# Kernel optimization log

Hardware: AMD Instinct MI355X
Metric: run time of the kernel (lower is better)

Reference implementation:

```python
import jax, jax.numpy as jnp
import numpy as np

B, C, NS, NT = 8, 256, 16384, 2048
KQ = 64            # self-attention key/query dim
D = 64             # cond_conv_feat_dim
W0, W1, W2 = D * D, D * D, D * 1   # dynamic weight sizes (predict_mask=True)
B0, B1, B2 = D, D, 1
CTRL = W0 + W1 + W2 + B0 + B1 + B2  # 8385


def setup_inputs() -> dict:
    key = jax.random.key(0)
    ks = jax.random.split(key, 9)
    return {
        "scene_feat": jax.random.normal(ks[0], (B, C, NS), jnp.float32),
        "template_feat": jax.random.normal(ks[1], (B, C, NT), jnp.float32),
        # SelfAttention 1x1-conv (= linear over channels) weights
        "q_w": jax.random.normal(ks[2], (KQ, C), jnp.float32) * 0.02,
        "k_w": jax.random.normal(ks[3], (KQ, C), jnp.float32) * 0.02,
        "v_w": jax.random.normal(ks[4], (C, C), jnp.float32) * 0.02,
        # projection head of SimpleAggregator: Conv1d(3*C -> D, k=1) + ReLU
        "proj_w": jax.random.normal(ks[5], (D, 3 * C), jnp.float32) * 0.02,
        "proj_b": jnp.zeros((D,), jnp.float32),
        # controller head: Linear(C -> CTRL), init normal(std=0.01), bias 0
        "ctrl_w": jax.random.normal(ks[6], (CTRL, C), jnp.float32) * 0.01,
        "ctrl_b": jnp.zeros((CTRL,), jnp.float32),
    }


def _self_attention(x, q_w, k_w, v_w):
    # x: [B, C, N] -> [B, C_out, N]
    q = jnp.einsum("kc,bcn->bnk", q_w, x)          # [B, N, KQ]
    k = jnp.einsum("kc,bcn->bkn", k_w, x)          # [B, KQ, N]
    v = jnp.einsum("oc,bcn->bno", v_w, x)          # [B, N, C_out]
    attn = jax.nn.softmax(jnp.einsum("bnk,bkm->bnm", q / jnp.sqrt(jnp.float32(KQ)), k), axis=-1)
    y = jnp.einsum("bnm,bmo->bon", attn, v)        # [B, C_out, N]
    return y


def reference(scene_feat, template_feat, q_w, k_w, v_w, proj_w, proj_b, ctrl_w, ctrl_b):
    # ---- SimpleAggregator (self-attention on template inside) ----
    t_sa = _self_attention(template_feat, q_w, k_w, v_w)       # [B, C, NT]
    t_max = jnp.max(t_sa, axis=-1, keepdims=True)              # [B, C, 1]
    aggr = jnp.concatenate(
        [scene_feat - t_max, scene_feat * t_max, scene_feat], axis=1
    )                                                          # [B, 3C, NS]
    x = jax.nn.relu(jnp.einsum("oc,bcn->bon", proj_w, aggr) + proj_b[None, :, None])  # [B, D, NS]

    # ---- controller head on ORIGINAL template_feat max-pooled ----
    pooled = jnp.max(template_feat, axis=-1)                   # [B, C]
    params = pooled @ ctrl_w.T + ctrl_b                        # [B, CTRL]

    # parse_dynamic_params: splits = weights then biases
    o = 0
    w0 = params[:, o:o + W0].reshape(B, D, D); o += W0
    w1 = params[:, o:o + W1].reshape(B, D, D); o += W1
    w2 = params[:, o:o + W2].reshape(B, 1, D); o += W2
    b0 = params[:, o:o + B0]; o += B0
    b1 = params[:, o:o + B1]; o += B1
    b2 = params[:, o:o + B2]

    # per-sample dynamic 1x1 convs (groups=batch trick == batched GEMM)
    x = jax.nn.relu(jnp.einsum("boi,bin->bon", w0, x) + b0[:, :, None])
    x = jax.nn.relu(jnp.einsum("boi,bin->bon", w1, x) + b1[:, :, None])
    x = jnp.einsum("boi,bin->bon", w2, x) + b2[:, :, None]    # [B, 1, NS], no relu (mask layer)
    return x.reshape(B, NS)
```

## Files before the change

### kernel.cpp

```cpp
#include <hip/hip_runtime.h>


typedef __attribute__((ext_vector_type(8))) short short8;
typedef __attribute__((ext_vector_type(4))) short short4v;
typedef __attribute__((ext_vector_type(4))) float f32x4;

__device__ __forceinline__ unsigned short f2bf(float f){
  unsigned u = __float_as_uint(f);
  u += 0x7FFFu + ((u >> 16) & 1u);
  return (unsigned short)(u >> 16);
}
__device__ __forceinline__ unsigned fenc(float f){
  unsigned u = __float_as_uint(f);
  return (u & 0x80000000u) ? ~u : (u | 0x80000000u);
}
__device__ __forceinline__ float fdec(unsigned k){
  unsigned u = (k & 0x80000000u) ? (k & 0x7FFFFFFFu) : ~k;
  return __uint_as_float(u);
}

__global__ __launch_bounds__(256) void k0w(const float* __restrict__ qw,
    const float* __restrict__ kw, const float* __restrict__ vw,
    unsigned short* __restrict__ Wbf, unsigned* __restrict__ tmaxe,
    unsigned* __restrict__ pooledEnc){
  if (blockIdx.x == 0){
    const unsigned ninf = fenc(-3.0e38f);
    for (int i = threadIdx.x; i < 2048; i += 256){
      tmaxe[i] = 0u;
      pooledEnc[i] = ninf;
    }
  }
  const int e = (blockIdx.x * 256 + threadIdx.x) * 4;
  const int row = e >> 8, c = e & 255;
  const float* src;
  float scl = 1.0f;
  if (row < 64){ src = qw + row * 256 + c; scl = 0.125f; }
  else if (row < 128){ src = kw + (row - 64) * 256 + c; }
  else { src = vw + (row - 128) * 256 + c; }
  float4 v = *(const float4*)src;
  short4v o;
  o[0] = (short)f2bf(v.x * scl); o[1] = (short)f2bf(v.y * scl);
  o[2] = (short)f2bf(v.z * scl); o[3] = (short)f2bf(v.w * scl);
  *(short4v*)(Wbf + e) = o;
}

__global__ __launch_bounds__(256) void k0_tt(const float* __restrict__ T,
    unsigned short* __restrict__ Tt, unsigned* __restrict__ pooledEnc){
  const int b = blockIdx.x, nt = blockIdx.y, ct = blockIdx.z;
  const int n0 = nt * 128, c0 = ct * 32;
  const int tid = threadIdx.x;
  __shared__ float Ls[32][129];
  const int cr = tid >> 3, nq = tid & 7;
  const float* src = T + ((size_t)b * 256 + c0 + cr) * 2048 + n0 + nq * 16;
  float4 v0 = ((const float4*)src)[0];
  float4 v1 = ((const float4*)src)[1];
  float4 v2 = ((const float4*)src)[2];
  float4 v3 = ((const float4*)src)[3];
  float mx = fmaxf(fmaxf(fmaxf(v0.x, v0.y), fmaxf(v0.z, v0.w)),
                   fmaxf(fmaxf(v1.x, v1.y), fmaxf(v1.z, v1.w)));
  mx = fmaxf(mx, fmaxf(fmaxf(fmaxf(v2.x, v2.y), fmaxf(v2.z, v2.w)),
                       fmaxf(fmaxf(v3.x, v3.y), fmaxf(v3.z, v3.w))));
  mx = fmaxf(mx, __shfl_xor(mx, 1));
  mx = fmaxf(mx, __shfl_xor(mx, 2));
  mx = fmaxf(mx, __shfl_xor(mx, 4));
  if (nq == 0) atomicMax(&pooledEnc[b * 256 + c0 + cr], fenc(mx));
  float* lr = &Ls[cr][nq * 16];
  *(float4*)lr = v0; *(float4*)(lr + 4) = v1;
  *(float4*)(lr + 8) = v2; *(float4*)(lr + 12) = v3;
  __syncthreads();
  const int nr = tid >> 1, ch = tid & 1;
  unsigned short ob[16];
  #pragma unroll
  for (int j = 0; j < 16; j++) ob[j] = f2bf(Ls[ch * 16 + j][nr]);
  unsigned short* dst = Tt + ((size_t)b * 2048 + n0 + nr) * 256 + c0 + ch * 16;
  *(short8*)dst = *(short8*)&ob[0];
  *(short8*)(dst + 8) = *(short8*)&ob[8];
}

__global__ __launch_bounds__(256) void k23_qkv_params(
    const unsigned short* __restrict__ Wbf, const unsigned short* __restrict__ Tt,
    unsigned short* __restrict__ qo, unsigned short* __restrict__ ko,
    unsigned short* __restrict__ vt,
    const unsigned* __restrict__ pooledEnc, const float* __restrict__ cw,
    const float* __restrict__ cb, float* __restrict__ params){
  const int wg = blockIdx.x;
  const int tid = threadIdx.x, lane = tid & 63, w = tid >> 6;
  if (wg >= 512){
    __shared__ float P[8 * 256];
    for (int i = tid; i < 2048; i += 256) P[i] = fdec(pooledEnc[i]);
    __syncthreads();
    const int r = (wg - 512) * 4 + w;
    if (r >= 8385) return;
    float4 c4 = ((const float4*)(cw + (size_t)r * 256))[lane];
    float bias = cb[r];
    #pragma unroll
    for (int b = 0; b < 8; b++){
      const float* pbp = P + b * 256 + lane * 4;
      float s = c4.x * pbp[0] + c4.y * pbp[1] + c4.z * pbp[2] + c4.w * pbp[3];
      #pragma unroll
      for (int d = 1; d < 64; d <<= 1) s += __shfl_xor(s, d);
      if (lane == 0) params[b * 8385 + r] = s + bias;
    }
    return;
  }
  const int b = wg & 7, nt = wg >> 3;
  const int n0 = nt * 32;
  const int l15 = lane & 15, g = lane >> 4;
  const unsigned short* Tb = Tt + (size_t)b * 2048 * 256;

  f32x4 aqk[2][2], av[4][2];
  #pragma unroll
  for (int i = 0; i < 2; i++)
    #pragma unroll
    for (int nf = 0; nf < 2; nf++) aqk[i][nf] = (f32x4){0.f,0.f,0.f,0.f};
  #pragma unroll
  for (int j = 0; j < 4; j++)
    #pragma unroll
    for (int nf = 0; nf < 2; nf++) av[j][nf] = (f32x4){0.f,0.f,0.f,0.f};

  #pragma unroll 2
  for (int kc = 0; kc < 8; kc++){
    short8 bfr[2];
    #pragma unroll
    for (int nf = 0; nf < 2; nf++)
      bfr[nf] = *(const short8*)(Tb + (size_t)(n0 + nf * 16 + l15) * 256 + kc * 32 + g * 8);
    short8 aq[2];
    #pragma unroll
    for (int i = 0; i < 2; i++)
      aq[i] = *(const short8*)(Wbf + (size_t)((2 * w + i) * 16 + l15) * 256 + kc * 32 + g * 8);
    short8 afv[4];
    #pragma unroll
    for (int j = 0; j < 4; j++)
      afv[j] = *(const short8*)(Wbf + (size_t)(128 + (4 * w + j) * 16 + l15) * 256 + kc * 32 + g * 8);
    #pragma unroll
    for (int i = 0; i < 2; i++)
      #pragma unroll
      for (int nf = 0; nf < 2; nf++)
        aqk[i][nf] = __builtin_amdgcn_mfma_f32_16x16x32_bf16(aq[i], bfr[nf], aqk[i][nf], 0, 0, 0);
    #pragma unroll
    for (int j = 0; j < 4; j++)
      #pragma unroll
      for (int nf = 0; nf < 2; nf++)
        av[j][nf] = __builtin_amdgcn_mfma_f32_16x16x32_bf16(bfr[nf], afv[j], av[j][nf], 0, 0, 0);
  }
  unsigned short* qk = (w < 2) ? qo : ko;
  #pragma unroll
  for (int i = 0; i < 2; i++)
    #pragma unroll
    for (int nf = 0; nf < 2; nf++){
      int n = n0 + nf * 16 + l15;
      int cbase = (w & 1) * 32 + i * 16 + g * 4;
      short4v pk;
      #pragma unroll
      for (int r = 0; r < 4; r++) pk[r] = (short)f2bf(aqk[i][nf][r]);
      *(short4v*)(qk + ((size_t)b * 2048 + n) * 64 + cbase) = pk;
    }
  #pragma unroll
  for (int j = 0; j < 4; j++)
    #pragma unroll
    for (int nf = 0; nf < 2; nf++){
      int o = (4 * w + j) * 16 + l15;
      int nb2 = n0 + nf * 16 + g * 4;
      short4v pv;
      #pragma unroll
      for (int r = 0; r < 4; r++) pv[r] = (short)f2bf(av[j][nf][r]);
      *(short4v*)(vt + ((size_t)b * 256 + o) * 2048 + nb2) = pv;
    }
}

__global__ __launch_bounds__(512, 4) void kA_scores(
    const unsigned short* __restrict__ Qg, const unsigned short* __restrict__ Kg,
    unsigned short* __restrict__ Pg, float* __restrict__ sbuf,
    int b0, int bshift){
  const int wg = blockIdx.x;
  const int bmask = (1 << bshift) - 1;
  const int b = b0 + (wg & bmask);
  const int q0 = (wg >> bshift) * 32;
  const int tid = threadIdx.x, lane = tid & 63, w = tid >> 6;
  const int l15 = lane & 15, g = lane >> 4;
  __shared__ float wsum[32][8];
  const unsigned short* Qb = Qg + (size_t)b * 2048 * 64;
  const unsigned short* Kb = Kg + (size_t)b * 2048 * 64;
  unsigned short* Pb = Pg + (size_t)(wg & bmask) * 2048 * 2048;

  short8 qf[2][2];
  #pragma unroll
  for (int qi = 0; qi < 2; qi++)
    #pragma unroll
    for (int kc = 0; kc < 2; kc++)
      qf[qi][kc] = *(const short8*)(Qb + (size_t)(q0 + qi * 16 + l15) * 64 + kc * 32 + g * 8);

  float ps[2] = {0.f, 0.f};

  const int wm0 = w * 256;
  #pragma unroll
  for (int mt = 0; mt < 4; ++mt){
    const int mb = wm0 + mt * 64;
    short8 kf[4][2];
    #pragma unroll
    for (int mi = 0; mi < 4; mi++)
      #pragma unroll
      for (int kc = 0; kc < 2; kc++)
        kf[mi][kc] = *(const short8*)(Kb + (size_t)(mb + mi * 16 + l15) * 64 + kc * 32 + g * 8);
    #pragma unroll
    for (int qi = 0; qi < 2; qi++){
      f32x4 sa[4];
      #pragma unroll
      for (int mi = 0; mi < 4; mi++) sa[mi] = (f32x4){0.f,0.f,0.f,0.f};
      #pragma unroll
      for (int mi = 0; mi < 4; mi++)
        #pragma unroll
        for (int kc = 0; kc < 2; kc++)
          sa[mi] = __builtin_amdgcn_mfma_f32_16x16x32_bf16(kf[mi][kc], qf[qi][kc], sa[mi], 0, 0, 0);
      #pragma unroll
      for (int mi = 0; mi < 4; mi++){
        short4v pk;
        #pragma unroll
        for (int r = 0; r < 4; r++){
          float p = __expf(sa[mi][r]);
          ps[qi] += p;
          pk[r] = (short)f2bf(p);
        }
        *(short4v*)(Pb + (size_t)(q0 + qi * 16 + l15) * 2048 + mb + mi * 16 + g * 4) = pk;
      }
    }
  }
  #pragma unroll
  for (int qi = 0; qi < 2; qi++){
    float t = ps[qi];
    t += __shfl_xor(t, 16);
    t += __shfl_xor(t, 32);
    if (lane < 16) wsum[qi * 16 + l15][w] = t;
  }
  __syncthreads();
  if (tid < 32){
    float t = 0.f;
    #pragma unroll
    for (int i = 0; i < 8; i++) t += wsum[tid][i];
    sbuf[(size_t)b * 2048 + q0 + tid] = t;
  }
}

__global__ __launch_bounds__(256, 3) void kB_pv(
    const unsigned short* __restrict__ Pg, const unsigned short* __restrict__ Vt,
    const float* __restrict__ sbuf, unsigned* __restrict__ tmaxe,
    int b0, int bshift){
  const int wg = blockIdx.x;
  const int bmask = (1 << bshift) - 1;
  const int b = b0 + (wg & bmask);
  const int rest = wg >> bshift;
  const int oh = rest & 1;
  const int n0 = (rest >> 1) * 64;
  const int tid = threadIdx.x, lane = tid & 63, w = tid >> 6;
  const int l15 = lane & 15, g = lane >> 4;
  __shared__ __align__(16) unsigned char smem[2][24576];

  const unsigned short* Pb = Pg + (size_t)(wg & bmask) * 2048 * 2048;
  const unsigned short* Vb = Vt + ((size_t)b * 256 + oh * 128) * 2048;

  f32x4 acc[4][2];
  #pragma unroll
  for (int ni = 0; ni < 4; ni++)
    #pragma unroll
    for (int oi = 0; oi < 2; oi++) acc[ni][oi] = (f32x4){0.f,0.f,0.f,0.f};

  const unsigned short* psrc[6];
  {
    #pragma unroll
    for (int k = 0; k < 6; k++){
      int d = k * 4096 + w * 1024 + lane * 16;
      if (k < 2){
        int row = d >> 7;
        int colB = (d & 127) ^ ((row & 7) << 4);
        psrc[k] = Pb + (size_t)(n0 + row) * 2048 + (colB >> 1);
      } else {
        int dv = d - 8192;
        int row = dv >> 7;
        int colB = (dv & 127) ^ ((row & 7) << 4);
        psrc[k] = Vb + (size_t)row * 2048 + (colB >> 1);
      }
    }
  }
  auto ISSUE = [&](int m0, int bufIdx){
    #pragma unroll
    for (int k = 0; k < 6; k++){
      unsigned char* dst = &smem[bufIdx][k * 4096 + w * 1024];
      __builtin_amdgcn_global_load_lds(
          (const __attribute__((address_space(1))) void*)(psrc[k] + m0),
          (__attribute__((address_space(3))) void*)dst, 16, 0, 0);
    }
  };

  ISSUE(0, 0);
  __syncthreads();

  for (int t = 0; t < 32; ++t){
    unsigned char* cur = smem[t & 1];
    if (t < 31) ISSUE((t + 1) * 64, (t + 1) & 1);
    short8 af[4][2], bf[2][2];
    #pragma unroll
    for (int ni = 0; ni < 4; ni++)
      #pragma unroll
      for (int kc = 0; kc < 2; kc++){
        int row = ni * 16 + l15;
        af[ni][kc] = *(const short8*)(cur + ((row * 128 + kc * 64 + g * 16) ^ ((row & 7) << 4)));
      }
    #pragma unroll
    for (int oi = 0; oi < 2; oi++)
      #pragma unroll
      for (int kc = 0; kc < 2; kc++){
        int row = w * 32 + oi * 16 + l15;
        bf[oi][kc] = *(const short8*)(cur + 8192 + ((row * 128 + kc * 64 + g * 16) ^ ((row & 7) << 4)));
      }
    #pragma unroll
    for (int ni = 0; ni < 4; ni++)
      #pragma unroll
      for (int oi = 0; oi < 2; oi++)
        #pragma unroll
        for (int kc = 0; kc < 2; kc++)
          acc[ni][oi] = __builtin_amdgcn_mfma_f32_16x16x32_bf16(af[ni][kc], bf[oi][kc], acc[ni][oi], 0, 0, 0);
    if (t < 31)
      __syncthreads();
  }
  float inv[4][4];
  #pragma unroll
  for (int ni = 0; ni < 4; ni++)
    #pragma unroll
    for (int r = 0; r < 4; r++)
      inv[ni][r] = 1.0f / sbuf[(size_t)b * 2048 + n0 + ni * 16 + g * 4 + r];
  #pragma unroll
  for (int oi = 0; oi < 2; oi++){
    float cm = -1e30f;
    #pragma unroll
    for (int ni = 0; ni < 4; ni++)
      #pragma unroll
      for (int r = 0; r < 4; r++)
        cm = fmaxf(cm, acc[ni][oi][r] * inv[ni][r]);
    cm = fmaxf(cm, __shfl_xor(cm, 16));
    cm = fmaxf(cm, __shfl_xor(cm, 32));
    if (lane < 16)
      atomicMax(&tmaxe[b * 256 + oh * 128 + w * 32 + oi * 16 + lane], fenc(cm));
  }
}

__global__ __launch_bounds__(256) void k5_weff(const float* __restrict__ proj_w,
    const float* __restrict__ proj_b, const unsigned* __restrict__ tmaxe,
    const float* __restrict__ params, unsigned short* __restrict__ weff,
    float* __restrict__ beff, unsigned short* __restrict__ w0b,
    unsigned short* __restrict__ w1b){
  const int b = blockIdx.y, o = blockIdx.x;
  const int c = threadIdx.x;
  float t = fdec(tmaxe[b * 256 + c]);
  float p0 = proj_w[o * 768 + c];
  float p1 = proj_w[o * 768 + 256 + c];
  float p2 = proj_w[o * 768 + 512 + c];
  weff[((size_t)b * 64 + o) * 256 + c] = f2bf(p0 + p1 * t + p2);
  float s = p0 * t;
  #pragma unroll
  for (int d = 1; d < 64; d <<= 1) s += __shfl_xor(s, d);
  __shared__ float sm[4];
  if ((c & 63) == 0) sm[c >> 6] = s;
  __syncthreads();
  if (c == 0) beff[b * 64 + o] = proj_b[o] - (sm[0] + sm[1] + sm[2] + sm[3]);
  if (c < 64)        w0b[((size_t)b * 64 + o) * 64 + c] = f2bf(params[b * 8385 + o * 64 + c]);
  else if (c < 128)  w1b[((size_t)b * 64 + o) * 64 + (c - 64)] = f2bf(params[b * 8385 + 4096 + o * 64 + (c - 64)]);
}

__global__ __launch_bounds__(512) void k6_main(const float* __restrict__ Sg,
    const unsigned short* __restrict__ weff, const float* __restrict__ beff,
    const unsigned short* __restrict__ w0b, const unsigned short* __restrict__ w1b,
    const float* __restrict__ params, float* __restrict__ out){
  const int b = blockIdx.y, nt = blockIdx.x;
  const int n0 = nt * 256;
  const int tid = threadIdx.x, lane = tid & 63, w = tid >> 6;
  const int l15 = lane & 15, g = lane >> 4;
  __shared__ __align__(16) unsigned char smem[65536];
  unsigned short* H0 = (unsigned short*)smem;
  unsigned char*  Ub = smem + 32768;
  unsigned short* H1 = (unsigned short*)Ub;

  const float* Sb = Sg + (size_t)b * 256 * 16384;
  const unsigned short* We = weff + (size_t)b * 64 * 256;
  f32x4 a0[4][2];
  #pragma unroll
  for (int mi = 0; mi < 4; mi++)
    #pragma unroll
    for (int ni = 0; ni < 2; ni++) a0[mi][ni] = (f32x4){0.f,0.f,0.f,0.f};

  const int scc = tid & 31;
  const int snb = (tid >> 5) * 16;
  const float* src0 = Sb + (size_t)scc * 16384 + n0 + snb;
  float4 v0 = ((const float4*)src0)[0];
  float4 v1 = ((const float4*)src0)[1];
  float4 v2 = ((const float4*)src0)[2];
  float4 v3 = ((const float4*)src0)[3];
  for (int k0 = 0; k0 < 256; k0 += 32){
    float vals[16] = {v0.x,v0.y,v0.z,v0.w, v1.x,v1.y,v1.z,v1.w,
                      v2.x,v2.y,v2.z,v2.w, v3.x,v3.y,v3.z,v3.w};
    #pragma unroll
    for (int j = 0; j < 16; j++){
      int n = snb + j;
      unsigned byteo = ((unsigned)(n * 64 + scc * 2)) ^ ((unsigned)((n >> 1) & 3) << 4);
      *(unsigned short*)(Ub + byteo) = f2bf(vals[j]);
    }
    if (k0 < 224){
      const float* nsrc = Sb + (size_t)(k0 + 32 + scc) * 16384 + n0 + snb;
      v0 = ((const float4*)nsrc)[0];
      v1 = ((const float4*)nsrc)[1];
      v2 = ((const float4*)nsrc)[2];
      v3 = ((const float4*)nsrc)[3];
    }
    __syncthreads();
    short8 bf0[2];
    #pragma unroll
    for (int ni = 0; ni < 2; ni++){
      int n = w * 32 + ni * 16 + l15;
      bf0[ni] = *(const short8*)(Ub + (((unsigned)(n * 64 + g * 16)) ^ ((unsigned)((n >> 1) & 3) << 4)));
    }
    #pragma unroll
    for (int mi = 0; mi < 4; mi++){
      short8 af = *(const short8*)(We + (mi * 16 + l15) * 256 + k0 + g * 8);
      #pragma unroll
      for (int ni = 0; ni < 2; ni++)
        a0[mi][ni] = __builtin_amdgcn_mfma_f32_16x16x32_bf16(af, bf0[ni], a0[mi][ni], 0, 0, 0);
    }
    __syncthreads();
  }
  const float* be = beff + b * 64;
  #pragma unroll
  for (int mi = 0; mi < 4; mi++)
    #pragma unroll
    for (int ni = 0; ni < 2; ni++){
      int n = w * 32 + ni * 16 + l15;
      unsigned base = ((unsigned)(n * 128 + mi * 32 + g * 8)) ^ ((unsigned)((n & 7) << 4));
      unsigned short hh[4];
      #pragma unroll
      for (int r = 0; r < 4; r++){
        int o = mi * 16 + g * 4 + r;
        hh[r] = f2bf(fmaxf(a0[mi][ni][r] + be[o], 0.f));
      }
      *(unsigned*)((unsigned char*)H0 + base)     = (unsigned)hh[0] | ((unsigned)hh[1] << 16);
      *(unsigned*)((unsigned char*)H0 + base + 4) = (unsigned)hh[2] | ((unsigned)hh[3] << 16);
    }
  __syncthreads();
  f32x4 a1[4][2];
  #pragma unroll
  for (int mi = 0; mi < 4; mi++)
    #pragma unroll
    for (int ni = 0; ni < 2; ni++) a1[mi][ni] = (f32x4){0.f,0.f,0.f,0.f};
  const unsigned short* W0 = w0b + (size_t)b * 4096;
  #pragma unroll
  for (int ks = 0; ks < 2; ks++){
    short8 bfh[2];
    #pragma unroll
    for (int ni = 0; ni < 2; ni++){
      int n = w * 32 + ni * 16 + l15;
      unsigned off = ((unsigned)(n * 128 + ks * 64 + g * 16)) ^ ((unsigned)((n & 7) << 4));
      bfh[ni] = *(const short8*)((unsigned char*)H0 + off);
    }
    #pragma unroll
    for (int mi = 0; mi < 4; mi++){
      short8 af = *(const short8*)(W0 + (mi * 16 + l15) * 64 + ks * 32 + g * 8);
      #pragma unroll
      for (int ni = 0; ni < 2; ni++)
        a1[mi][ni] = __builtin_amdgcn_mfma_f32_16x16x32_bf16(af, bfh[ni], a1[mi][ni], 0, 0, 0);
    }
  }
  const float* pp = params + (size_t)b * 8385;
  const float* b0p = pp + 8256;
  #pragma unroll
  for (int mi = 0; mi < 4; mi++)
    #pragma unroll
    for (int ni = 0; ni < 2; ni++){
      int n = w * 32 + ni * 16 + l15;
      unsigned base = ((unsigned)(n * 128 + mi * 32 + g * 8)) ^ ((unsigned)((n & 7) << 4));
      unsigned short hh[4];
      #pragma unroll
      for (int r = 0; r < 4; r++){
        int o = mi * 16 + g * 4 + r;
        hh[r] = f2bf(fmaxf(a1[mi][ni][r] + b0p[o], 0.f));
      }
      *(unsigned*)((unsigned char*)H1 + base)     = (unsigned)hh[0] | ((unsigned)hh[1] << 16);
      *(unsigned*)((unsigned char*)H1 + base + 4) = (unsigned)hh[2] | ((unsigned)hh[3] << 16);
    }
  __syncthreads();
  f32x4 a2[4][2];
  #pragma unroll
  for (int mi = 0; mi < 4; mi++)
    #pragma unroll
    for (int ni = 0; ni < 2; ni++) a2[mi][ni] = (f32x4){0.f,0.f,0.f,0.f};
  const unsigned short* W1 = w1b + (size_t)b * 4096;
  #pragma unroll
  for (int ks = 0; ks < 2; ks++){
    short8 bfh[2];
    #pragma unroll
    for (int ni = 0; ni < 2; ni++){
      int n = w * 32 + ni * 16 + l15;
      unsigned off = ((unsigned)(n * 128 + ks * 64 + g * 16)) ^ ((unsigned)((n & 7) << 4));
      bfh[ni] = *(const short8*)((unsigned char*)H1 + off);
    }
    #pragma unroll
    for (int mi = 0; mi < 4; mi++){
      short8 af = *(const short8*)(W1 + (mi * 16 + l15) * 64 + ks * 32 + g * 8);
      #pragma unroll
      for (int ni = 0; ni < 2; ni++)
        a2[mi][ni] = __builtin_amdgcn_mfma_f32_16x16x32_bf16(af, bfh[ni], a2[mi][ni], 0, 0, 0);
    }
  }
  const float* b1p = pp + 8320;
  const float* w2p = pp + 8192;
  float b2v = pp[8384];
  #pragma unroll
  for (int ni = 0; ni < 2; ni++){
    float t = 0.f;
    #pragma unroll
    for (int mi = 0; mi < 4; mi++)
      #pragma unroll
      for (int r = 0; r < 4; r++){
        int o = mi * 16 + g * 4 + r;
        t += w2p[o] * fmaxf(a2[mi][ni][r] + b1p[o], 0.f);
      }
    t += __shfl_xor(t, 16);
    t += __shfl_xor(t, 32);
    if (lane < 16)
      out[(size_t)b * 16384 + n0 + w * 32 + ni * 16 + l15] = t + b2v;
  }
}

extern "C" void kernel_launch(void* const* d_in, const int* in_sizes, int n_in,
                              void* d_out, int out_size, void* d_ws, size_t ws_size,
                              hipStream_t stream){
  const float* scene = (const float*)d_in[0];
  const float* tmpl  = (const float*)d_in[1];
  const float* qw    = (const float*)d_in[2];
  const float* kw    = (const float*)d_in[3];
  const float* vw    = (const float*)d_in[4];
  const float* pw    = (const float*)d_in[5];
  const float* pb    = (const float*)d_in[6];
  const float* cw    = (const float*)d_in[7];
  const float* cb    = (const float*)d_in[8];
  float* out = (float*)d_out;
  char* ws = (char*)d_ws;

  unsigned short* Q      = (unsigned short*)(ws + 0);
  unsigned short* K      = (unsigned short*)(ws + (2u << 20));
  unsigned short* V      = (unsigned short*)(ws + (4u << 20));
  unsigned*       pooledEnc = (unsigned*)(ws + (12u << 20));
  unsigned*       tmaxe  = (unsigned*)(ws + (12u << 20) + 8192);
  float*          params = (float*)(ws + (12u << 20) + 16384);
  unsigned short* w0b    = (unsigned short*)(ws + (13u << 20));
  unsigned short* w1b    = (unsigned short*)(ws + (13u << 20) + 65536);
  unsigned short* weff   = (unsigned short*)(ws + (13u << 20) + 131072);
  float*          beff   = (float*)(ws + (13u << 20) + 131072 + 262144);
  float*          sbuf   = (float*)(ws + (14u << 20));
  unsigned short* Wbf    = (unsigned short*)(ws + (14u << 20) + 131072);
  unsigned short* Pbuf   = (unsigned short*)(ws + (16u << 20));
  unsigned short* Tt     = Pbuf;

  const size_t pPerBatch = (size_t)2048 * 2048 * 2;
  size_t avail = ws_size > (16u << 20) ? ws_size - (16u << 20) : 0;
  int nb = 8, bshift = 3;
  while (nb > 1 && (size_t)nb * pPerBatch > avail){ nb >>= 1; bshift--; }

  k0w<<<dim3(96), dim3(256), 0, stream>>>(qw, kw, vw, Wbf, tmaxe, pooledEnc);
  k0_tt<<<dim3(8, 16, 8), dim3(256), 0, stream>>>(tmpl, Tt, pooledEnc);
  k23_qkv_params<<<dim3(512 + 2097), dim3(256), 0, stream>>>(Wbf, Tt, Q, K, V,
                                                             pooledEnc, cw, cb, params);
  for (int b0 = 0; b0 < 8; b0 += nb){
    kA_scores<<<dim3(64 * nb), dim3(512), 0, stream>>>(Q, K, Pbuf, sbuf, b0, bshift);
    kB_pv<<<dim3(64 * nb), dim3(256), 0, stream>>>(Pbuf, V, sbuf, tmaxe, b0, bshift);
  }
  k5_weff<<<dim3(64, 8), dim3(256), 0, stream>>>(pw, pb, tmaxe, params, weff, beff, w0b, w1b);
  k6_main<<<dim3(64, 8), dim3(512), 0, stream>>>(scene, weff, beff, w0b, w1b, params, out);
}
```

Before: 140.4 us.

## Store attention probabilities and V in FP8 and use FP8 MFMA for PV

The unnormalized attention probabilities and the transposed V are now written as FP8 e4m3 instead of bf16, and the PV kernel loads them at half the size and multiplies with the fp8 MFMA instruction. This halves the traffic of the large 2048x2048 per-batch P matrix and the LDS staging footprint, which allows higher occupancy. It also means more batches fit in the workspace at once. The cost is lower accuracy in the softmax-weighted sum. exp scores above the e4m3 range (448) could saturate, and small probabilities lose precision.

```diff
diff --git a/kernel.cpp b/kernel.cpp
--- a/kernel.cpp
+++ b/kernel.cpp
@@ -1,4 +1,5 @@
 #include <hip/hip_runtime.h>
+#include <hip/hip_fp8.h>
 
 
 typedef __attribute__((ext_vector_type(8))) short short8;
@@ -9,6 +10,9 @@
   unsigned u = __float_as_uint(f);
   u += 0x7FFFu + ((u >> 16) & 1u);
   return (unsigned short)(u >> 16);
+}
+__device__ __forceinline__ unsigned char f2e4m3(float f){
+  return __hip_fp8_e4m3(f).__x;
 }
 __device__ __forceinline__ unsigned fenc(float f){
   unsigned u = __float_as_uint(f);
@@ -80,7 +84,7 @@
 __global__ __launch_bounds__(256) void k23_qkv_params(
     const unsigned short* __restrict__ Wbf, const unsigned short* __restrict__ Tt,
     unsigned short* __restrict__ qo, unsigned short* __restrict__ ko,
-    unsigned short* __restrict__ vt,
+    unsigned char* __restrict__ vt8,
     const unsigned* __restrict__ pooledEnc, const float* __restrict__ cw,
     const float* __restrict__ cb, float* __restrict__ params){
   const int wg = blockIdx.x;
@@ -161,16 +165,17 @@
     for (int nf = 0; nf < 2; nf++){
       int o = (4 * w + j) * 16 + l15;
       int nb2 = n0 + nf * 16 + g * 4;
-      short4v pv;
-      #pragma unroll
-      for (int r = 0; r < 4; r++) pv[r] = (short)f2bf(av[j][nf][r]);
-      *(short4v*)(vt + ((size_t)b * 256 + o) * 2048 + nb2) = pv;
+      unsigned pv8 = 0;
+      #pragma unroll
+      for (int r = 0; r < 4; r++)
+        pv8 |= (unsigned)f2e4m3(av[j][nf][r]) << (8 * r);
+      *(unsigned*)(vt8 + ((size_t)b * 256 + o) * 2048 + nb2) = pv8;
     }
 }
 
 __global__ __launch_bounds__(512, 4) void kA_scores(
     const unsigned short* __restrict__ Qg, const unsigned short* __restrict__ Kg,
-    unsigned short* __restrict__ Pg, float* __restrict__ sbuf,
+    unsigned char* __restrict__ Pg, float* __restrict__ sbuf,
     int b0, int bshift){
   const int wg = blockIdx.x;
   const int bmask = (1 << bshift) - 1;
@@ -181,7 +186,7 @@
   __shared__ float wsum[32][8];
   const unsigned short* Qb = Qg + (size_t)b * 2048 * 64;
   const unsigned short* Kb = Kg + (size_t)b * 2048 * 64;
-  unsigned short* Pb = Pg + (size_t)(wg & bmask) * 2048 * 2048;
+  unsigned char* Pb = Pg + (size_t)(wg & bmask) * 2048 * 2048;
 
   short8 qf[2][2];
   #pragma unroll
@@ -214,14 +219,14 @@
           sa[mi] = __builtin_amdgcn_mfma_f32_16x16x32_bf16(kf[mi][kc], qf[qi][kc], sa[mi], 0, 0, 0);
       #pragma unroll
       for (int mi = 0; mi < 4; mi++){
-        short4v pk;
+        unsigned pk8 = 0;
         #pragma unroll
         for (int r = 0; r < 4; r++){
           float p = __expf(sa[mi][r]);
           ps[qi] += p;
-          pk[r] = (short)f2bf(p);
+          pk8 |= (unsigned)f2e4m3(p) << (8 * r);
         }
-        *(short4v*)(Pb + (size_t)(q0 + qi * 16 + l15) * 2048 + mb + mi * 16 + g * 4) = pk;
+        *(unsigned*)(Pb + (size_t)(q0 + qi * 16 + l15) * 2048 + mb + mi * 16 + g * 4) = pk8;
       }
     }
   }
@@ -241,8 +246,8 @@
   }
 }
 
-__global__ __launch_bounds__(256, 3) void kB_pv(
-    const unsigned short* __restrict__ Pg, const unsigned short* __restrict__ Vt,
+__global__ __launch_bounds__(256, 4) void kB_pv(
+    const unsigned char* __restrict__ Pg, const unsigned char* __restrict__ Vt,
     const float* __restrict__ sbuf, unsigned* __restrict__ tmaxe,
     int b0, int bshift){
   const int wg = blockIdx.x;
@@ -253,10 +258,10 @@
   const int n0 = (rest >> 1) * 64;
   const int tid = threadIdx.x, lane = tid & 63, w = tid >> 6;
   const int l15 = lane & 15, g = lane >> 4;
-  __shared__ __align__(16) unsigned char smem[2][24576];
-
-  const unsigned short* Pb = Pg + (size_t)(wg & bmask) * 2048 * 2048;
-  const unsigned short* Vb = Vt + ((size_t)b * 256 + oh * 128) * 2048;
+  __shared__ __align__(16) unsigned char smem[2][12288];
+
+  const unsigned char* Pb = Pg + (size_t)(wg & bmask) * 2048 * 2048;
+  const unsigned char* Vb = Vt + ((size_t)b * 256 + oh * 128) * 2048;
 
   f32x4 acc[4][2];
   #pragma unroll
@@ -264,26 +269,26 @@
     #pragma unroll
     for (int oi = 0; oi < 2; oi++) acc[ni][oi] = (f32x4){0.f,0.f,0.f,0.f};
 
-  const unsigned short* psrc[6];
+  const unsigned char* psrc[3];
   {
     #pragma unroll
-    for (int k = 0; k < 6; k++){
+    for (int k = 0; k < 3; k++){
       int d = k * 4096 + w * 1024 + lane * 16;
-      if (k < 2){
-        int row = d >> 7;
-        int colB = (d & 127) ^ ((row & 7) << 4);
-        psrc[k] = Pb + (size_t)(n0 + row) * 2048 + (colB >> 1);
+      if (k < 1){
+        int row = d >> 6;
+        int colB = (d & 63) ^ ((row & 3) << 4);
+        psrc[k] = Pb + (size_t)(n0 + row) * 2048 + colB;
       } else {
-        int dv = d - 8192;
-        int row = dv >> 7;
-        int colB = (dv & 127) ^ ((row & 7) << 4);
-        psrc[k] = Vb + (size_t)row * 2048 + (colB >> 1);
+        int dv = d - 4096;
+        int row = dv >> 6;
+        int colB = (dv & 63) ^ ((row & 3) << 4);
+        psrc[k] = Vb + (size_t)row * 2048 + colB;
       }
     }
   }
   auto ISSUE = [&](int m0, int bufIdx){
     #pragma unroll
-    for (int k = 0; k < 6; k++){
+    for (int k = 0; k < 3; k++){
       unsigned char* dst = &smem[bufIdx][k * 4096 + w * 1024];
       __builtin_amdgcn_global_load_lds(
           (const __attribute__((address_space(1))) void*)(psrc[k] + m0),
@@ -297,20 +302,20 @@
   for (int t = 0; t < 32; ++t){
     unsigned char* cur = smem[t & 1];
     if (t < 31) ISSUE((t + 1) * 64, (t + 1) & 1);
-    short8 af[4][2], bf[2][2];
+    long af[4][2], bf[2][2];
     #pragma unroll
     for (int ni = 0; ni < 4; ni++)
       #pragma unroll
       for (int kc = 0; kc < 2; kc++){
         int row = ni * 16 + l15;
-        af[ni][kc] = *(const short8*)(cur + ((row * 128 + kc * 64 + g * 16) ^ ((row & 7) << 4)));
+        af[ni][kc] = *(const long*)(cur + row * 64 + ((kc * 32 + g * 8) ^ ((row & 3) << 4)));
       }
     #pragma unroll
     for (int oi = 0; oi < 2; oi++)
       #pragma unroll
       for (int kc = 0; kc < 2; kc++){
         int row = w * 32 + oi * 16 + l15;
-        bf[oi][kc] = *(const short8*)(cur + 8192 + ((row * 128 + kc * 64 + g * 16) ^ ((row & 7) << 4)));
+        bf[oi][kc] = *(const long*)(cur + 4096 + row * 64 + ((kc * 32 + g * 8) ^ ((row & 3) << 4)));
       }
     #pragma unroll
     for (int ni = 0; ni < 4; ni++)
@@ -318,7 +323,7 @@
       for (int oi = 0; oi < 2; oi++)
         #pragma unroll
         for (int kc = 0; kc < 2; kc++)
-          acc[ni][oi] = __builtin_amdgcn_mfma_f32_16x16x32_bf16(af[ni][kc], bf[oi][kc], acc[ni][oi], 0, 0, 0);
+          acc[ni][oi] = __builtin_amdgcn_mfma_f32_16x16x32_fp8_fp8(af[ni][kc], bf[oi][kc], acc[ni][oi], 0, 0, 0);
     if (t < 31)
       __syncthreads();
   }
@@ -544,7 +549,7 @@
 
   unsigned short* Q      = (unsigned short*)(ws + 0);
   unsigned short* K      = (unsigned short*)(ws + (2u << 20));
-  unsigned short* V      = (unsigned short*)(ws + (4u << 20));
+  unsigned char*  V8     = (unsigned char*)(ws + (4u << 20));
   unsigned*       pooledEnc = (unsigned*)(ws + (12u << 20));
   unsigned*       tmaxe  = (unsigned*)(ws + (12u << 20) + 8192);
   float*          params = (float*)(ws + (12u << 20) + 16384);
@@ -554,21 +559,21 @@
   float*          beff   = (float*)(ws + (13u << 20) + 131072 + 262144);
   float*          sbuf   = (float*)(ws + (14u << 20));
   unsigned short* Wbf    = (unsigned short*)(ws + (14u << 20) + 131072);
-  unsigned short* Pbuf   = (unsigned short*)(ws + (16u << 20));
-  unsigned short* Tt     = Pbuf;
-
-  const size_t pPerBatch = (size_t)2048 * 2048 * 2;
+  unsigned char*  P8buf  = (unsigned char*)(ws + (16u << 20));
+  unsigned short* Tt     = (unsigned short*)P8buf;
+
+  const size_t pPerBatch = (size_t)2048 * 2048;
   size_t avail = ws_size > (16u << 20) ? ws_size - (16u << 20) : 0;
   int nb = 8, bshift = 3;
   while (nb > 1 && (size_t)nb * pPerBatch > avail){ nb >>= 1; bshift--; }
 
   k0w<<<dim3(96), dim3(256), 0, stream>>>(qw, kw, vw, Wbf, tmaxe, pooledEnc);
   k0_tt<<<dim3(8, 16, 8), dim3(256), 0, stream>>>(tmpl, Tt, pooledEnc);
-  k23_qkv_params<<<dim3(512 + 2097), dim3(256), 0, stream>>>(Wbf, Tt, Q, K, V,
+  k23_qkv_params<<<dim3(512 + 2097), dim3(256), 0, stream>>>(Wbf, Tt, Q, K, V8,
                                                              pooledEnc, cw, cb, params);
   for (int b0 = 0; b0 < 8; b0 += nb){
-    kA_scores<<<dim3(64 * nb), dim3(512), 0, stream>>>(Q, K, Pbuf, sbuf, b0, bshift);
-    kB_pv<<<dim3(64 * nb), dim3(256), 0, stream>>>(Pbuf, V, sbuf, tmaxe, b0, bshift);
+    kA_scores<<<dim3(64 * nb), dim3(512), 0, stream>>>(Q, K, P8buf, sbuf, b0, bshift);
+    kB_pv<<<dim3(64 * nb), dim3(256), 0, stream>>>(P8buf, V8, sbuf, tmaxe, b0, bshift);
   }
   k5_weff<<<dim3(64, 8), dim3(256), 0, stream>>>(pw, pb, tmaxe, params, weff, beff, w0b, w1b);
   k6_main<<<dim3(64, 8), dim3(512), 0, stream>>>(scene, weff, beff, w0b, w1b, params, out);
```

Result: no change. 140.1 us (-0.2%).
